# Kernel optimization log

Hardware: AMD Instinct MI355X
Metric: run time of the kernel (lower is better)

Reference implementation:

```python
import jax, jax.numpy as jnp
import numpy as np

H = 128          # h_dim
N_NODES = 100000
N_EDGES = 1600000
N_GRAPHS = 256
EPS_BN = 1e-5


def setup_inputs() -> dict:
    key = jax.random.key(0)
    ks = jax.random.split(key, 12)
    x = jax.random.normal(ks[0], (N_NODES, 4), dtype=jnp.float32)
    edge_index = jax.random.randint(ks[1], (2, N_EDGES), 0, N_NODES, dtype=jnp.int64)
    batch = jnp.sort(jax.random.randint(ks[2], (N_NODES,), 0, N_GRAPHS, dtype=jnp.int64))
    # Linear weights (xavier-ish scale), stored as [in, out]
    W1 = jax.random.normal(ks[3], (4, H), dtype=jnp.float32) * (1.0 / np.sqrt(4))
    W2 = jax.random.normal(ks[4], (H, H), dtype=jnp.float32) * (1.0 / np.sqrt(H))
    W3 = jax.random.normal(ks[5], (H, H), dtype=jnp.float32) * (1.0 / np.sqrt(H))
    Wfc = jax.random.normal(ks[6], (H, 1), dtype=jnp.float32) * (1.0 / np.sqrt(H))
    def bn_params(k):
        k1, k2, k3, k4 = jax.random.split(k, 4)
        gamma = 1.0 + 0.1 * jax.random.normal(k1, (H,), dtype=jnp.float32)
        beta = 0.1 * jax.random.normal(k2, (H,), dtype=jnp.float32)
        mean = 0.1 * jax.random.normal(k3, (H,), dtype=jnp.float32)
        var = 1.0 + 0.1 * jax.random.uniform(k4, (H,), dtype=jnp.float32)
        return gamma, beta, mean, var
    g1, b1, m1, v1 = bn_params(ks[7])
    g2, b2, m2, v2 = bn_params(ks[8])
    g3, b3, m3, v3 = bn_params(ks[9])
    return {
        "x": x, "edge_index": edge_index, "batch": batch,
        "W1": W1, "g1": g1, "b1": b1, "m1": m1, "v1": v1,
        "W2": W2, "g2": g2, "b2": b2, "m2": m2, "v2": v2,
        "W3": W3, "g3": g3, "b3": b3, "m3": m3, "v3": v3,
        "Wfc": Wfc,
    }


def _gin_layer(h, src, dst, W, gamma, beta, mean, var):
    # GINConv with eps=0: mlp(x + sum_{j in N(i)} x_j)
    aggr = jax.ops.segment_sum(h[src], dst, num_segments=N_NODES)
    z = (h + aggr) @ W                                  # Linear(bias=False)
    z = (z - mean) * (gamma / jnp.sqrt(var + EPS_BN)) + beta  # BatchNorm1d (eval)
    return jax.nn.relu(z)


def reference(x, edge_index, batch,
              W1, g1, b1, m1, v1,
              W2, g2, b2, m2, v2,
              W3, g3, b3, m3, v3,
              Wfc):
    src, dst = edge_index[0], edge_index[1]
    h = _gin_layer(x, src, dst, W1, g1, b1, m1, v1)
    h = _gin_layer(h, src, dst, W2, g2, b2, m2, v2)
    h = _gin_layer(h, src, dst, W3, g3, b3, m3, v3)
    # dropout: identity in eval mode
    sums = jax.ops.segment_sum(h, batch, num_segments=N_GRAPHS)      # [G, H]
    cnts = jax.ops.segment_sum(jnp.ones((N_NODES, 1), h.dtype), batch,
                               num_segments=N_GRAPHS)                # [G, 1]
    pooled = sums / jnp.maximum(cnts, 1.0)
    return jax.nn.sigmoid(pooled @ Wfc)                               # [G, 1]
```

## Files before the change

kernel.cpp:

```cpp
#include <hip/hip_runtime.h>
#include <hip/hip_fp8.h>
#include <math.h>

#define N_NODES 100000
#define N_EDGES 1600000
#define N_GRAPHS 256
#define H 128
#define EPS_BN 1e-5f
#define ELLW 64

#define PSZ 256
#define PSH 8
#define P_PART 391
#define BLD_NBLK 200
#define EPT 32
#define EPB_A (256 * EPT)

typedef unsigned int uint;
typedef unsigned short ushort;
typedef __attribute__((ext_vector_type(8))) short bf16x8;
typedef __attribute__((ext_vector_type(4))) float f32x4;
typedef __attribute__((ext_vector_type(2))) float f32x2;
typedef __attribute__((ext_vector_type(4))) int i32x4;
typedef __attribute__((ext_vector_type(2))) int i32x2;

__device__ __forceinline__ uint f2bf_bits(float x) {
    uint u = __float_as_uint(x);
    return (u + 0x7fffu + ((u >> 16) & 1u)) >> 16;
}
__device__ __forceinline__ uint pack_bf2(float a, float b) {
    return f2bf_bits(a) | (f2bf_bits(b) << 16);
}

__device__ __forceinline__ unsigned char f32_to_fp8(float x) {
#if __has_builtin(__builtin_amdgcn_cvt_pk_fp8_f32)
    int v = __builtin_amdgcn_cvt_pk_fp8_f32(x, 0.0f, 0, false);
    return (unsigned char)(v & 0xff);
#else
    __hip_fp8_e4m3 q(x);
    return (unsigned char)q.__x;
#endif
}
__device__ __forceinline__ f32x4 fp8x4_to_f32x4(uint v) {
    f32x4 r;
#if __has_builtin(__builtin_amdgcn_cvt_pk_f32_fp8)
    f32x2 lo = __builtin_amdgcn_cvt_pk_f32_fp8((int)v, false);
    f32x2 hi = __builtin_amdgcn_cvt_pk_f32_fp8((int)v, true);
    r.x = lo.x; r.y = lo.y; r.z = hi.x; r.w = hi.y;
#else
    __hip_fp8_e4m3 a, b, c, d;
    a.__x = (unsigned char)(v & 0xff);
    b.__x = (unsigned char)((v >> 8) & 0xff);
    c.__x = (unsigned char)((v >> 16) & 0xff);
    d.__x = (unsigned char)((v >> 24) & 0xff);
    r.x = (float)a; r.y = (float)b; r.z = (float)c; r.w = (float)d;
#endif
    return r;
}

__global__ __launch_bounds__(256) void k_hist(const int* __restrict__ dst,
                                              int* __restrict__ hist,
                                              const int* __restrict__ batch,
                                              int* __restrict__ gstart,
                                              const float* __restrict__ W2,
                                              ushort* __restrict__ Wpk2,
                                              const float* __restrict__ W3,
                                              ushort* __restrict__ Wpk3,
                                              float* __restrict__ Gz,
                                              uint* __restrict__ HfApad,
                                              uint* __restrict__ HfBpad) {
    __shared__ int h[P_PART];
    int b = blockIdx.x;
    if (b < BLD_NBLK) {
        for (int i = threadIdx.x; i < P_PART; i += 256) h[i] = 0;
        __syncthreads();
        int base = b * EPB_A + threadIdx.x * EPT;
        #pragma unroll
        for (int j = 0; j < EPT / 4; j++) {
            int e = base + j * 4;
            if (e + 4 <= N_EDGES) {
                i32x4 d = __builtin_nontemporal_load((const i32x4*)&dst[e]);
                atomicAdd(&h[d.x >> PSH], 1);
                atomicAdd(&h[d.y >> PSH], 1);
                atomicAdd(&h[d.z >> PSH], 1);
                atomicAdd(&h[d.w >> PSH], 1);
            }
        }
        __syncthreads();
        for (int i = threadIdx.x; i < P_PART; i += 256)
            hist[b * P_PART + i] = h[i];
        return;
    }
    if (b < 592) {
        int n = (b - 200) * 256 + threadIdx.x;
        if (n >= N_NODES) return;
        int g = batch[n];
        int gp = (n == 0) ? -1 : batch[n - 1];
        for (int gr = gp + 1; gr <= g; gr++) gstart[gr] = n;
        if (n == N_NODES - 1) {
            for (int gr = g + 1; gr <= N_GRAPHS; gr++) gstart[gr] = N_NODES;
        }
        return;
    }
    if (b >= 608) {
        if (threadIdx.x < N_GRAPHS) Gz[threadIdx.x] = 0.0f;
        if (threadIdx.x < 32) HfApad[threadIdx.x] = 0u;
        if (threadIdx.x < 32) HfBpad[threadIdx.x] = 0u;
        return;
    }
    const float* W = (b < 600) ? W2 : W3;
    ushort* Wpk = (b < 600) ? Wpk2 : Wpk3;
    int t = ((b < 600) ? (b - 592) : (b - 600)) * 256 + threadIdx.x;
    int lane = t & 63, nt = (t >> 6) & 7, kt = t >> 9;
    int n = nt * 16 + (lane & 15);
    int kbase = kt * 32 + (lane >> 4) * 8;
    ushort v[8];
    #pragma unroll
    for (int j = 0; j < 8; j++)
        v[j] = (ushort)f2bf_bits(W[(size_t)(kbase + j) * H + n]);
    uint4 pk;
    pk.x = (uint)v[0] | ((uint)v[1] << 16);
    pk.y = (uint)v[2] | ((uint)v[3] << 16);
    pk.z = (uint)v[4] | ((uint)v[5] << 16);
    pk.w = (uint)v[6] | ((uint)v[7] << 16);
    *(uint4*)&Wpk[(size_t)t * 8] = pk;
}

__global__ __launch_bounds__(256) void k_scan_a(const int* __restrict__ hist,
                                                int* __restrict__ offs,
                                                int* __restrict__ tot) {
    __shared__ int lds[256];
    int p = blockIdx.x;
    int t = threadIdx.x;
    int v = (t < BLD_NBLK) ? hist[t * P_PART + p] : 0;
    lds[t] = v;
    __syncthreads();
    for (int off = 1; off < 256; off <<= 1) {
        int tmp = (t >= off) ? lds[t - off] : 0;
        __syncthreads();
        lds[t] += tmp;
        __syncthreads();
    }
    if (t < BLD_NBLK) offs[t * P_PART + p] = lds[t] - v;
    if (t == 255) tot[p] = lds[255];
}

__global__ void k_scan_b(const int* __restrict__ tot, int* __restrict__ parr) {
    __shared__ int lds[512];
    int p = threadIdx.x;
    int v = (p < P_PART) ? tot[p] : 0;
    lds[p] = v;
    __syncthreads();
    for (int off = 1; off < 512; off <<= 1) {
        int tmp = (p >= off) ? lds[p - off] : 0;
        __syncthreads();
        lds[p] += tmp;
        __syncthreads();
    }
    if (p < P_PART) parr[p] = lds[p] - v;
    if (p == 0) parr[P_PART] = N_EDGES;
}

__global__ __launch_bounds__(256) void k_scatter(const int* __restrict__ src,
                                                 const int* __restrict__ dst,
                                                 const int* __restrict__ offs,
                                                 const int* __restrict__ parr,
                                                 i32x2* __restrict__ ebuf) {
    __shared__ int lofs[P_PART];
    for (int i = threadIdx.x; i < P_PART; i += 256)
        lofs[i] = offs[blockIdx.x * P_PART + i] + parr[i];
    __syncthreads();
    int base = blockIdx.x * EPB_A + threadIdx.x * EPT;
    #pragma unroll
    for (int j = 0; j < EPT / 4; j++) {
        int e = base + j * 4;
        if (e + 4 <= N_EDGES) {
            i32x4 d = __builtin_nontemporal_load((const i32x4*)&dst[e]);
            i32x4 s = __builtin_nontemporal_load((const i32x4*)&src[e]);
            #pragma unroll
            for (int k = 0; k < 4; k++) {
                int dk = (k == 0) ? d.x : (k == 1) ? d.y : (k == 2) ? d.z : d.w;
                int sk = (k == 0) ? s.x : (k == 1) ? s.y : (k == 2) ? s.z : s.w;
                int pos = atomicAdd(&lofs[dk >> PSH], 1);
                i32x2 sd; sd.x = sk; sd.y = dk;
                ebuf[pos] = sd;
            }
        }
    }
}

__global__ __launch_bounds__(256) void k_build(const i32x2* __restrict__ ebuf,
                                               const int* __restrict__ parr,
                                               int* __restrict__ cnt,
                                               int* __restrict__ ell) {
    __shared__ int lc[PSZ];
    int p = blockIdx.x;
    for (int i = threadIdx.x; i < PSZ; i += 256) lc[i] = 0;
    __syncthreads();
    int e0 = parr[p], e1 = parr[p + 1];
    for (int i = e0 + threadIdx.x; i < e1; i += 256) {
        i32x2 sd = ebuf[i];
        int d = sd.y;
        int slot = atomicAdd(&lc[d & (PSZ - 1)], 1);
        if (slot < ELLW) ell[(size_t)d * ELLW + slot] = sd.x;
    }
    __syncthreads();
    int nb = p * PSZ;
    for (int i = threadIdx.x; i < PSZ; i += 256) {
        int n = nb + i;
        if (n < N_NODES) {
            int c = lc[i];
            cnt[n] = c;
            int cc = (c < ELLW) ? c : ELLW;
            int cp = (cc + 15) & ~15;
            if (cp > ELLW) cp = ELLW;
            for (int slot = cc; slot < cp; slot++)
                ell[(size_t)n * ELLW + slot] = N_NODES;
        }
    }
}

__global__ __launch_bounds__(256) void k_layer1(
    const float* __restrict__ x, const int* __restrict__ cnt,
    const int* __restrict__ ell, const float* __restrict__ W1,
    const float* __restrict__ gamma, const float* __restrict__ beta,
    const float* __restrict__ mean, const float* __restrict__ var,
    uint* __restrict__ Hf8) {
    __shared__ float scs[128], shs[128];
    int tid = threadIdx.x;
    if (tid < 128) {
        float sc = gamma[tid] * rsqrtf(var[tid] + EPS_BN);
        scs[tid] = sc;
        shs[tid] = beta[tid] - mean[tid] * sc;
    }
    __syncthreads();
    int lane = tid & 63, wave = tid >> 6;
    int sub = lane >> 4, m = lane & 15;
    int n = blockIdx.x * 16 + wave * 4 + sub;
    if (n >= N_NODES) return;
    int cn = cnt[n]; if (cn > ELLW) cn = ELLW;
    const int* row = &ell[(size_t)n * ELLW];
    float4 acc = {0.f, 0.f, 0.f, 0.f};
    for (int e = m; e < cn; e += 16) {
        float4 v = *(const float4*)&x[(size_t)row[e] * 4];
        acc.x += v.x; acc.y += v.y; acc.z += v.z; acc.w += v.w;
    }
    #pragma unroll
    for (int off = 8; off > 0; off >>= 1) {
        acc.x += __shfl_down(acc.x, off, 16);
        acc.y += __shfl_down(acc.y, off, 16);
        acc.z += __shfl_down(acc.z, off, 16);
        acc.w += __shfl_down(acc.w, off, 16);
    }
    int src = lane & 48;
    float4 xs = *(const float4*)&x[(size_t)n * 4];
    float uu[4];
    uu[0] = __shfl(acc.x, src, 64) + xs.x;
    uu[1] = __shfl(acc.y, src, 64) + xs.y;
    uu[2] = __shfl(acc.z, src, 64) + xs.z;
    uu[3] = __shfl(acc.w, src, 64) + xs.w;
    int j0 = m * 8;
    float z[8] = {0.f, 0.f, 0.f, 0.f, 0.f, 0.f, 0.f, 0.f};
    #pragma unroll
    for (int k = 0; k < 4; k++) {
        float4 wa = *(const float4*)&W1[k * H + j0];
        float4 wb = *(const float4*)&W1[k * H + j0 + 4];
        z[0] += uu[k] * wa.x; z[1] += uu[k] * wa.y;
        z[2] += uu[k] * wa.z; z[3] += uu[k] * wa.w;
        z[4] += uu[k] * wb.x; z[5] += uu[k] * wb.y;
        z[6] += uu[k] * wb.z; z[7] += uu[k] * wb.w;
    }
    #pragma unroll
    for (int i = 0; i < 8; i++)
        z[i] = fmaxf(z[i] * scs[j0 + i] + shs[j0 + i], 0.0f);
    uint2 q;
    q.x = (uint)f32_to_fp8(z[0]) | ((uint)f32_to_fp8(z[1]) << 8)
        | ((uint)f32_to_fp8(z[2]) << 16) | ((uint)f32_to_fp8(z[3]) << 24);
    q.y = (uint)f32_to_fp8(z[4]) | ((uint)f32_to_fp8(z[5]) << 8)
        | ((uint)f32_to_fp8(z[6]) << 16) | ((uint)f32_to_fp8(z[7]) << 24);
    *(uint2*)&Hf8[(size_t)n * 32 + m * 2] = q;
}

__global__ __launch_bounds__(256) void k_aggr_gemm(
    const uint* __restrict__ Hin, const int* __restrict__ cnt,
    const int* __restrict__ ell, const uint* __restrict__ Wpk,
    const float* __restrict__ gamma, const float* __restrict__ beta,
    const float* __restrict__ mean, const float* __restrict__ var,
    unsigned char* __restrict__ Hout,
    const int* __restrict__ batch, const float* __restrict__ Wfc,
    float* __restrict__ Gz, int mode) {
    __shared__ uint lds_u[64 * 68];
    __shared__ float wfc[128];
    __shared__ int bb[64];
    __shared__ float sblk[64];
    int tid = threadIdx.x;
    int row0 = blockIdx.x * 64;
    if (mode == 2) {
        if (tid < 128) wfc[tid] = Wfc[tid];
        if (tid < 64) {
            int rr = row0 + tid;
            bb[tid] = (rr < N_NODES) ? batch[rr] : -1;
        }
    }
    int wave = tid >> 6, lane = tid & 63;
    int g = lane >> 4, c8 = lane & 15;
    int n0 = row0 + wave * 16;

    int cnt16 = 0;
    if (lane < 16) {
        int nn = n0 + lane;
        cnt16 = (nn < N_NODES) ? cnt[nn] : 0;
    }
    int npre = (n0 < N_NODES) ? n0 : (N_NODES - 1);
    i32x4 idp = *(const i32x4*)(ell + (size_t)npre * ELLW + 4 * g);

    for (int i = 0; i < 16; i++) {
        int n = n0 + i;
        bool valid = (n < N_NODES);
        int cn = __shfl(cnt16, i, 64);
        if (cn > ELLW) cn = ELLW;
        int cnp = (cn + 15) & ~15;
        const int* row = ell + (size_t)(valid ? n : (N_NODES - 1)) * ELLW;
        i32x4 id = idp;
        if (i < 15) {
            int n2 = n + 1; if (n2 >= N_NODES) n2 = N_NODES - 1;
            idp = *(const i32x4*)(ell + (size_t)n2 * ELLW + 4 * g);
        }
        uint2 sp = {0u, 0u};
        if (g == 0 && valid) sp = *(const uint2*)&Hin[(size_t)n * 32 + c8 * 2];

        f32x4 A = {0.f, 0.f, 0.f, 0.f};
        f32x4 B = {0.f, 0.f, 0.f, 0.f};
        for (int e = 0; e < cnp; e += 16) {
            i32x4 idn = id;
            if (e + 16 < cnp) idn = *(const i32x4*)(row + e + 16 + 4 * g);
            int s0 = id.x, s1 = id.y, s2 = id.z, s3 = id.w;
            uint2 p0 = *(const uint2*)&Hin[(size_t)s0 * 32 + c8 * 2];
            uint2 p1 = *(const uint2*)&Hin[(size_t)s1 * 32 + c8 * 2];
            uint2 p2 = *(const uint2*)&Hin[(size_t)s2 * 32 + c8 * 2];
            uint2 p3 = *(const uint2*)&Hin[(size_t)s3 * 32 + c8 * 2];
            f32x4 l0 = fp8x4_to_f32x4(p0.x), h0 = fp8x4_to_f32x4(p0.y);
            f32x4 l1 = fp8x4_to_f32x4(p1.x), h1 = fp8x4_to_f32x4(p1.y);
            f32x4 l2 = fp8x4_to_f32x4(p2.x), h2 = fp8x4_to_f32x4(p2.y);
            f32x4 l3 = fp8x4_to_f32x4(p3.x), h3 = fp8x4_to_f32x4(p3.y);
            A += (l0 + l1) + (l2 + l3);
            B += (h0 + h1) + (h2 + h3);
            id = idn;
        }
        if (g == 0) {
            A += fp8x4_to_f32x4(sp.x);
            B += fp8x4_to_f32x4(sp.y);
        }
        #pragma unroll
        for (int off = 32; off >= 16; off >>= 1) {
            A.x += __shfl_down(A.x, off, 64);
            A.y += __shfl_down(A.y, off, 64);
            A.z += __shfl_down(A.z, off, 64);
            A.w += __shfl_down(A.w, off, 64);
            B.x += __shfl_down(B.x, off, 64);
            B.y += __shfl_down(B.y, off, 64);
            B.z += __shfl_down(B.z, off, 64);
            B.w += __shfl_down(B.w, off, 64);
        }
        if (g == 0) {
            uint4 ov;
            ov.x = pack_bf2(A.x, A.y);
            ov.y = pack_bf2(A.z, A.w);
            ov.z = pack_bf2(B.x, B.y);
            ov.w = pack_bf2(B.z, B.w);
            *(uint4*)&lds_u[(wave * 16 + i) * 68 + c8 * 4] = ov;
        }
    }

    int m = c8, quad = g;
    bf16x8 a[4];
    #pragma unroll
    for (int kt = 0; kt < 4; kt++)
        a[kt] = *(const bf16x8*)&lds_u[(wave * 16 + m) * 68 + kt * 16 + quad * 4];

    f32x4 acc[8];
    #pragma unroll
    for (int nt = 0; nt < 8; nt++) acc[nt] = (f32x4){0.f, 0.f, 0.f, 0.f};

    #pragma unroll
    for (int nt = 0; nt < 8; nt++) {
        #pragma unroll
        for (int kt = 0; kt < 4; kt++) {
            bf16x8 b = *(const bf16x8*)&Wpk[((size_t)(kt * 8 + nt) * 64 + lane) * 4];
            acc[nt] = __builtin_amdgcn_mfma_f32_16x16x32_bf16(a[kt], b, acc[nt], 0, 0, 0);
        }
    }

    if (mode == 1) {
        #pragma unroll
        for (int nt = 0; nt < 8; nt++) {
            int col = nt * 16 + m;
            float sc = gamma[col] * rsqrtf(var[col] + EPS_BN);
            float sh = beta[col] - mean[col] * sc;
            #pragma unroll
            for (int r = 0; r < 4; r++) {
                int row = row0 + wave * 16 + quad * 4 + r;
                if (row < N_NODES) {
                    float z = fmaxf(acc[nt][r] * sc + sh, 0.0f);
                    Hout[(size_t)row * 128 + col] = f32_to_fp8(z);
                }
            }
        }
    } else {
        float pr[4] = {0.f, 0.f, 0.f, 0.f};
        #pragma unroll
        for (int nt = 0; nt < 8; nt++) {
            int col = nt * 16 + m;
            float sc = gamma[col] * rsqrtf(var[col] + EPS_BN);
            float sh = beta[col] - mean[col] * sc;
            float wf = wfc[col];
            #pragma unroll
            for (int r = 0; r < 4; r++) {
                float z = fmaxf(acc[nt][r] * sc + sh, 0.0f);
                pr[r] += z * wf;
            }
        }
        #pragma unroll
        for (int r = 0; r < 4; r++) {
            float p = pr[r];
            p += __shfl_down(p, 8, 16);
            p += __shfl_down(p, 4, 16);
            p += __shfl_down(p, 2, 16);
            p += __shfl_down(p, 1, 16);
            if (m == 0) sblk[wave * 16 + quad * 4 + r] = p;
        }
        __syncthreads();
        if (tid == 0) {
            int i = 0;
            while (i < 64 && row0 + i < N_NODES) {
                int gg = bb[i];
                float s = 0.0f;
                while (i < 64 && row0 + i < N_NODES && bb[i] == gg) {
                    s += sblk[i]; i++;
                }
                atomicAdd(&Gz[gg], s);
            }
        }
    }
}

__global__ void k_fc(const float* __restrict__ Gz, const int* __restrict__ gstart,
                     float* __restrict__ out) {
    int g = threadIdx.x;
    if (g < N_GRAPHS) {
        int c = gstart[g + 1] - gstart[g];
        float z = Gz[g] / fmaxf((float)c, 1.0f);
        out[g] = 1.0f / (1.0f + expf(-z));
    }
}

extern "C" void kernel_launch(void* const* d_in, const int* in_sizes, int n_in,
                              void* d_out, int out_size, void* d_ws, size_t ws_size,
                              hipStream_t stream) {
    const float* x     = (const float*)d_in[0];
    const int*   ei    = (const int*)d_in[1];
    const int*   batch = (const int*)d_in[2];
    const float* W1    = (const float*)d_in[3];
    const float* g1    = (const float*)d_in[4];
    const float* b1    = (const float*)d_in[5];
    const float* m1    = (const float*)d_in[6];
    const float* v1    = (const float*)d_in[7];
    const float* W2    = (const float*)d_in[8];
    const float* g2    = (const float*)d_in[9];
    const float* b2    = (const float*)d_in[10];
    const float* m2    = (const float*)d_in[11];
    const float* v2    = (const float*)d_in[12];
    const float* W3    = (const float*)d_in[13];
    const float* g3    = (const float*)d_in[14];
    const float* b3    = (const float*)d_in[15];
    const float* m3    = (const float*)d_in[16];
    const float* v3    = (const float*)d_in[17];
    const float* Wfc   = (const float*)d_in[18];
    float* out = (float*)d_out;

    const int* srcp = ei;
    const int* dstp = ei + N_EDGES;

    uint* HfB  = (uint*)d_ws;
    uint* HfA  = HfB + (size_t)N_NODES * 32 + 32;
    int* cnt   = (int*)(HfA + (size_t)N_NODES * 32 + 32);
    int* ell   = cnt + N_NODES;
    int* gstart = ell + (size_t)N_NODES * ELLW;
    ushort* Wpk2 = (ushort*)(gstart + 260);
    ushort* Wpk3 = Wpk2 + 16384;
    int* hist  = (int*)(Wpk3 + 16384);
    int* offs  = hist + BLD_NBLK * P_PART;
    int* parr  = offs + BLD_NBLK * P_PART;
    int* tot   = parr + 400;
    float* Gz  = (float*)(tot + 400);
    i32x2* ebuf = (i32x2*)HfB;
    uint* HfApad = HfA + (size_t)N_NODES * 32;
    uint* HfBpad = HfB + (size_t)N_NODES * 32;

    k_hist<<<609, 256, 0, stream>>>(dstp, hist, batch, gstart, W2, Wpk2, W3, Wpk3,
                                    Gz, HfApad, HfBpad);
    k_scan_a<<<P_PART, 256, 0, stream>>>(hist, offs, tot);
    k_scan_b<<<1, 512, 0, stream>>>(tot, parr);
    k_scatter<<<BLD_NBLK, 256, 0, stream>>>(srcp, dstp, offs, parr, ebuf);
    k_build<<<P_PART, 256, 0, stream>>>(ebuf, parr, cnt, ell);

    k_layer1<<<(N_NODES + 15) / 16, 256, 0, stream>>>(
        x, cnt, ell, W1, g1, b1, m1, v1, HfA);
    k_aggr_gemm<<<(N_NODES + 63) / 64, 256, 0, stream>>>(
        HfA, cnt, ell, (const uint*)Wpk2, g2, b2, m2, v2,
        (unsigned char*)HfB, batch, Wfc, Gz, 1);
    k_aggr_gemm<<<(N_NODES + 63) / 64, 256, 0, stream>>>(
        HfB, cnt, ell, (const uint*)Wpk3, g3, b3, m3, v3,
        (unsigned char*)HfA, batch, Wfc, Gz, 2);
    k_fc<<<1, 256, 0, stream>>>(Gz, gstart, out);
}
```

Baseline: 287.2 us.

## Assign one node per wave in aggregation and shrink GEMM tile to eight rows

The aggregate-plus-GEMM kernel no longer has each wave gather 16 nodes one after another. It now launches 512-thread blocks covering 8 nodes, with each wave gathering one node in parallel. After a barrier, wave 0 alone runs the MFMA on a 16-row tile of which only 8 rows are used, and writes the results or pooled partial sums. The aim is more memory-level parallelism for the latency-bound neighbor gather. In exchange, half of the MFMA work is wasted, weight reloads per node double, seven waves sit idle during the GEMM, and the LDS batch grouping is replaced by per-quad atomics.

```diff
diff --git a/kernel.cpp b/kernel.cpp
--- a/kernel.cpp
+++ b/kernel.cpp
@@ -281,7 +281,7 @@
     *(uint2*)&Hf8[(size_t)n * 32 + m * 2] = q;
 }
 
-__global__ __launch_bounds__(256) void k_aggr_gemm(
+__global__ __launch_bounds__(512) void k_aggr_gemm(
     const uint* __restrict__ Hin, const int* __restrict__ cnt,
     const int* __restrict__ ell, const uint* __restrict__ Wpk,
     const float* __restrict__ gamma, const float* __restrict__ beta,
@@ -289,94 +289,69 @@
     unsigned char* __restrict__ Hout,
     const int* __restrict__ batch, const float* __restrict__ Wfc,
     float* __restrict__ Gz, int mode) {
-    __shared__ uint lds_u[64 * 68];
-    __shared__ float wfc[128];
-    __shared__ int bb[64];
-    __shared__ float sblk[64];
+    __shared__ uint lds_u[16 * 68];
     int tid = threadIdx.x;
-    int row0 = blockIdx.x * 64;
-    if (mode == 2) {
-        if (tid < 128) wfc[tid] = Wfc[tid];
-        if (tid < 64) {
-            int rr = row0 + tid;
-            bb[tid] = (rr < N_NODES) ? batch[rr] : -1;
-        }
-    }
-    int wave = tid >> 6, lane = tid & 63;
+    int wid = tid >> 6, lane = tid & 63;
+    int n0 = blockIdx.x * 8;
+    int n = n0 + wid;
+
     int g = lane >> 4, c8 = lane & 15;
-    int n0 = row0 + wave * 16;
-
-    int cnt16 = 0;
-    if (lane < 16) {
-        int nn = n0 + lane;
-        cnt16 = (nn < N_NODES) ? cnt[nn] : 0;
-    }
-    int npre = (n0 < N_NODES) ? n0 : (N_NODES - 1);
-    i32x4 idp = *(const i32x4*)(ell + (size_t)npre * ELLW + 4 * g);
-
-    for (int i = 0; i < 16; i++) {
-        int n = n0 + i;
-        bool valid = (n < N_NODES);
-        int cn = __shfl(cnt16, i, 64);
-        if (cn > ELLW) cn = ELLW;
-        int cnp = (cn + 15) & ~15;
-        const int* row = ell + (size_t)(valid ? n : (N_NODES - 1)) * ELLW;
-        i32x4 id = idp;
-        if (i < 15) {
-            int n2 = n + 1; if (n2 >= N_NODES) n2 = N_NODES - 1;
-            idp = *(const i32x4*)(ell + (size_t)n2 * ELLW + 4 * g);
-        }
-        uint2 sp = {0u, 0u};
-        if (g == 0 && valid) sp = *(const uint2*)&Hin[(size_t)n * 32 + c8 * 2];
-
-        f32x4 A = {0.f, 0.f, 0.f, 0.f};
-        f32x4 B = {0.f, 0.f, 0.f, 0.f};
-        for (int e = 0; e < cnp; e += 16) {
-            i32x4 idn = id;
-            if (e + 16 < cnp) idn = *(const i32x4*)(row + e + 16 + 4 * g);
-            int s0 = id.x, s1 = id.y, s2 = id.z, s3 = id.w;
-            uint2 p0 = *(const uint2*)&Hin[(size_t)s0 * 32 + c8 * 2];
-            uint2 p1 = *(const uint2*)&Hin[(size_t)s1 * 32 + c8 * 2];
-            uint2 p2 = *(const uint2*)&Hin[(size_t)s2 * 32 + c8 * 2];
-            uint2 p3 = *(const uint2*)&Hin[(size_t)s3 * 32 + c8 * 2];
-            f32x4 l0 = fp8x4_to_f32x4(p0.x), h0 = fp8x4_to_f32x4(p0.y);
-            f32x4 l1 = fp8x4_to_f32x4(p1.x), h1 = fp8x4_to_f32x4(p1.y);
-            f32x4 l2 = fp8x4_to_f32x4(p2.x), h2 = fp8x4_to_f32x4(p2.y);
-            f32x4 l3 = fp8x4_to_f32x4(p3.x), h3 = fp8x4_to_f32x4(p3.y);
-            A += (l0 + l1) + (l2 + l3);
-            B += (h0 + h1) + (h2 + h3);
-            id = idn;
-        }
-        if (g == 0) {
-            A += fp8x4_to_f32x4(sp.x);
-            B += fp8x4_to_f32x4(sp.y);
-        }
-        #pragma unroll
-        for (int off = 32; off >= 16; off >>= 1) {
-            A.x += __shfl_down(A.x, off, 64);
-            A.y += __shfl_down(A.y, off, 64);
-            A.z += __shfl_down(A.z, off, 64);
-            A.w += __shfl_down(A.w, off, 64);
-            B.x += __shfl_down(B.x, off, 64);
-            B.y += __shfl_down(B.y, off, 64);
-            B.z += __shfl_down(B.z, off, 64);
-            B.w += __shfl_down(B.w, off, 64);
-        }
-        if (g == 0) {
-            uint4 ov;
-            ov.x = pack_bf2(A.x, A.y);
-            ov.y = pack_bf2(A.z, A.w);
-            ov.z = pack_bf2(B.x, B.y);
-            ov.w = pack_bf2(B.z, B.w);
-            *(uint4*)&lds_u[(wave * 16 + i) * 68 + c8 * 4] = ov;
-        }
-    }
-
-    int m = c8, quad = g;
+    const int* row = &ell[(size_t)n * ELLW];
+    i32x4 id = *(const i32x4*)(row + 4 * g);
+    uint2 sp = {0u, 0u};
+    if (g == 0) sp = *(const uint2*)&Hin[(size_t)n * 32 + c8 * 2];
+    int cn = cnt[n]; if (cn > ELLW) cn = ELLW;
+    int cnp = (cn + 15) & ~15; if (cnp > ELLW) cnp = ELLW;
+
+    f32x4 A = {0.f, 0.f, 0.f, 0.f};
+    f32x4 B = {0.f, 0.f, 0.f, 0.f};
+    for (int e = 0; e < cnp; e += 16) {
+        i32x4 idn = id;
+        if (e + 16 < cnp) idn = *(const i32x4*)(row + e + 16 + 4 * g);
+        int s0 = id.x, s1 = id.y, s2 = id.z, s3 = id.w;
+        uint2 p0 = *(const uint2*)&Hin[(size_t)s0 * 32 + c8 * 2];
+        uint2 p1 = *(const uint2*)&Hin[(size_t)s1 * 32 + c8 * 2];
+        uint2 p2 = *(const uint2*)&Hin[(size_t)s2 * 32 + c8 * 2];
+        uint2 p3 = *(const uint2*)&Hin[(size_t)s3 * 32 + c8 * 2];
+        f32x4 l0 = fp8x4_to_f32x4(p0.x), h0 = fp8x4_to_f32x4(p0.y);
+        f32x4 l1 = fp8x4_to_f32x4(p1.x), h1 = fp8x4_to_f32x4(p1.y);
+        f32x4 l2 = fp8x4_to_f32x4(p2.x), h2 = fp8x4_to_f32x4(p2.y);
+        f32x4 l3 = fp8x4_to_f32x4(p3.x), h3 = fp8x4_to_f32x4(p3.y);
+        A += (l0 + l1) + (l2 + l3);
+        B += (h0 + h1) + (h2 + h3);
+        id = idn;
+    }
+    if (g == 0) {
+        A += fp8x4_to_f32x4(sp.x);
+        B += fp8x4_to_f32x4(sp.y);
+    }
+    #pragma unroll
+    for (int off = 32; off >= 16; off >>= 1) {
+        A.x += __shfl_down(A.x, off, 64);
+        A.y += __shfl_down(A.y, off, 64);
+        A.z += __shfl_down(A.z, off, 64);
+        A.w += __shfl_down(A.w, off, 64);
+        B.x += __shfl_down(B.x, off, 64);
+        B.y += __shfl_down(B.y, off, 64);
+        B.z += __shfl_down(B.z, off, 64);
+        B.w += __shfl_down(B.w, off, 64);
+    }
+    if (g == 0) {
+        uint4 ov;
+        ov.x = pack_bf2(A.x, A.y);
+        ov.y = pack_bf2(A.z, A.w);
+        ov.z = pack_bf2(B.x, B.y);
+        ov.w = pack_bf2(B.z, B.w);
+        *(uint4*)&lds_u[wid * 68 + c8 * 4] = ov;
+    }
+    __syncthreads();
+    if (wid != 0) return;
+
+    int m = lane & 15, quad = lane >> 4;
     bf16x8 a[4];
     #pragma unroll
     for (int kt = 0; kt < 4; kt++)
-        a[kt] = *(const bf16x8*)&lds_u[(wave * 16 + m) * 68 + kt * 16 + quad * 4];
+        a[kt] = *(const bf16x8*)&lds_u[m * 68 + kt * 16 + quad * 4];
 
     f32x4 acc[8];
     #pragma unroll
@@ -392,17 +367,17 @@
     }
 
     if (mode == 1) {
-        #pragma unroll
-        for (int nt = 0; nt < 8; nt++) {
-            int col = nt * 16 + m;
-            float sc = gamma[col] * rsqrtf(var[col] + EPS_BN);
-            float sh = beta[col] - mean[col] * sc;
+        if (quad < 2) {
             #pragma unroll
-            for (int r = 0; r < 4; r++) {
-                int row = row0 + wave * 16 + quad * 4 + r;
-                if (row < N_NODES) {
+            for (int nt = 0; nt < 8; nt++) {
+                int col = nt * 16 + m;
+                float sc = gamma[col] * rsqrtf(var[col] + EPS_BN);
+                float sh = beta[col] - mean[col] * sc;
+                #pragma unroll
+                for (int r = 0; r < 4; r++) {
+                    int rowi = n0 + quad * 4 + r;
                     float z = fmaxf(acc[nt][r] * sc + sh, 0.0f);
-                    Hout[(size_t)row * 128 + col] = f32_to_fp8(z);
+                    Hout[(size_t)rowi * 128 + col] = f32_to_fp8(z);
                 }
             }
         }
@@ -413,7 +388,7 @@
             int col = nt * 16 + m;
             float sc = gamma[col] * rsqrtf(var[col] + EPS_BN);
             float sh = beta[col] - mean[col] * sc;
-            float wf = wfc[col];
+            float wf = Wfc[col];
             #pragma unroll
             for (int r = 0; r < 4; r++) {
                 float z = fmaxf(acc[nt][r] * sc + sh, 0.0f);
@@ -422,24 +397,22 @@
         }
         #pragma unroll
         for (int r = 0; r < 4; r++) {
-            float p = pr[r];
-            p += __shfl_down(p, 8, 16);
-            p += __shfl_down(p, 4, 16);
-            p += __shfl_down(p, 2, 16);
-            p += __shfl_down(p, 1, 16);
-            if (m == 0) sblk[wave * 16 + quad * 4 + r] = p;
-        }
-        __syncthreads();
-        if (tid == 0) {
-            int i = 0;
-            while (i < 64 && row0 + i < N_NODES) {
-                int gg = bb[i];
-                float s = 0.0f;
-                while (i < 64 && row0 + i < N_NODES && bb[i] == gg) {
-                    s += sblk[i]; i++;
-                }
-                atomicAdd(&Gz[gg], s);
+            pr[r] += __shfl_down(pr[r], 8, 16);
+            pr[r] += __shfl_down(pr[r], 4, 16);
+            pr[r] += __shfl_down(pr[r], 2, 16);
+            pr[r] += __shfl_down(pr[r], 1, 16);
+        }
+        if (m == 0 && quad < 2) {
+            int base = n0 + quad * 4;
+            int gprev = batch[base];
+            float s = pr[0];
+            #pragma unroll
+            for (int r = 1; r < 4; r++) {
+                int gg = batch[base + r];
+                if (gg == gprev) s += pr[r];
+                else { atomicAdd(&Gz[gprev], s); gprev = gg; s = pr[r]; }
             }
+            atomicAdd(&Gz[gprev], s);
         }
     }
 }
@@ -506,10 +479,10 @@
 
     k_layer1<<<(N_NODES + 15) / 16, 256, 0, stream>>>(
         x, cnt, ell, W1, g1, b1, m1, v1, HfA);
-    k_aggr_gemm<<<(N_NODES + 63) / 64, 256, 0, stream>>>(
+    k_aggr_gemm<<<N_NODES / 8, 512, 0, stream>>>(
         HfA, cnt, ell, (const uint*)Wpk2, g2, b2, m2, v2,
         (unsigned char*)HfB, batch, Wfc, Gz, 1);
-    k_aggr_gemm<<<(N_NODES + 63) / 64, 256, 0, stream>>>(
+    k_aggr_gemm<<<N_NODES / 8, 512, 0, stream>>>(
         HfB, cnt, ell, (const uint*)Wpk3, g3, b3, m3, v3,
         (unsigned char*)HfA, batch, Wfc, Gz, 2);
     k_fc<<<1, 256, 0, stream>>>(Gz, gstart, out);
```

New measurement: 352.8 us. 1.23x slower.
